# Kernel tuning notes

Measured on AMD Instinct MI355X. Metric: run time of the kernel, lower is better.

Reference implementation:

```python
import jax, jax.numpy as jnp
import numpy as np
from math import sqrt

D_MODEL, N_H, D_H, D_CQ, D_CKV, D_HR = 2048, 16, 128, 768, 512, 64
B, S = 1, 2048


def _rope_cos_sin(seq_len, dim, base=10000.0):
    inv_freq = 1.0 / (base ** (jnp.arange(0, dim, 2, dtype=jnp.float32) / dim))
    ang = jnp.arange(seq_len, dtype=jnp.float32)[:, None] * inv_freq[None, :]  # (S, dim//2)
    return jnp.cos(ang), jnp.sin(ang)


def _rope(t, cos, sin):
    # t: (B, S, ..., dim) with sequence on axis 1; interleaved complex pairs
    shp = t.shape
    d2 = shp[-1] // 2
    tr = t.reshape(shp[:-1] + (d2, 2))
    x0, x1 = tr[..., 0], tr[..., 1]
    bshape = (1, shp[1]) + (1,) * (x0.ndim - 3) + (d2,)
    cs, sn = cos.reshape(bshape), sin.reshape(bshape)
    return jnp.stack([x0 * cs - x1 * sn, x0 * sn + x1 * cs], axis=-1).reshape(shp)


def setup_inputs() -> dict:
    key = jax.random.key(0)
    ks = jax.random.split(key, 10)
    sc = 0.02
    inp = {
        "x": jax.random.normal(ks[0], (B, S, D_MODEL), jnp.float32),
        "mask": jnp.triu(jnp.ones((S, S), dtype=bool), k=1),  # True -> masked (causal)
        "w_norm": jnp.ones((D_MODEL,), jnp.float32),
        "w_cq": jax.random.normal(ks[1], (D_MODEL, D_CQ), jnp.float32) * sc,
        "w_q": jax.random.normal(ks[2], (D_CQ, N_H * D_H), jnp.float32) * sc,
        "w_qr": jax.random.normal(ks[3], (D_CQ, N_H * D_HR), jnp.float32) * sc,
        "w_ckv": jax.random.normal(ks[4], (D_MODEL, D_CKV), jnp.float32) * sc,
        "w_k": jax.random.normal(ks[5], (D_CKV, N_H * D_H), jnp.float32) * sc,
        "w_kr": jax.random.normal(ks[6], (D_MODEL, D_HR), jnp.float32) * sc,
        "w_v": jax.random.normal(ks[7], (D_CKV, D_MODEL), jnp.float32) * sc,
        "w_o": jax.random.normal(ks[8], (N_H * D_H, D_MODEL), jnp.float32) * sc,
    }
    return inp


def reference(x, mask, w_norm, w_cq, w_q, w_qr, w_ckv, w_k, w_kr, w_v, w_o):
    b, s, _ = x.shape
    eps = jnp.finfo(x.dtype).eps
    h = x * jax.lax.rsqrt(jnp.mean(x * x, axis=-1, keepdims=True) + eps) * w_norm  # RMSNorm
    cos, sin = _rope_cos_sin(s, D_HR)

    c_q = h @ w_cq  # (b, s, d_c_q)
    q_c = (c_q @ w_q).reshape(b, s, N_H, D_H).transpose(0, 2, 1, 3)          # (b, h, s, d_h)
    q_r = _rope((c_q @ w_qr).reshape(b, s, N_H, D_HR), cos, sin).transpose(0, 2, 1, 3)
    q = jnp.concatenate([q_c, q_r], axis=-1)  # (b, h, s, d_h + d_h_R)

    c_kv = h @ w_ckv  # (b, s, d_c_kv)
    k_c = (c_kv @ w_k).reshape(b, s, N_H, D_H).transpose(0, 2, 1, 3)
    k_r = _rope(h @ w_kr, cos, sin)[:, None]  # (b, 1, s, d_h_R), shared across heads
    k = jnp.concatenate([k_c, jnp.broadcast_to(k_r, (b, N_H, s, D_HR))], axis=-1)
    v = (c_kv @ w_v).reshape(b, s, N_H, D_H).transpose(0, 2, 1, 3)

    score = jnp.einsum('bhqd,bhkd->bhqk', q, k) / sqrt(D_H + D_HR)
    score = jnp.where(mask, -jnp.inf, score)
    attn = jax.nn.softmax(score, axis=-1)
    out = jnp.einsum('bhqk,bhkd->bhqd', attn, v)  # (b, h, s, d_h)
    out = out.transpose(0, 2, 1, 3).reshape(b, s, N_H * D_H) @ w_o
    return x + out
```

## Files before the change

### kernel.cpp

```cpp
#include <hip/hip_runtime.h>
#include <hip/hip_bf16.h>
#include <math.h>

#define D_MODEL 2048
#define N_H     16
#define D_H     128
#define D_CQ    768
#define D_CKV   512
#define D_HR    64
#define SEQ     2048
#define N_ACT1  1408
#define NSPLIT  4

typedef short bf16x8 __attribute__((ext_vector_type(8)));
typedef float f32x4  __attribute__((ext_vector_type(4)));

__device__ inline short f2bf(float f) {
  union { float f; unsigned u; } v; v.f = f;
  unsigned r = (v.u + 0x7fff + ((v.u >> 16) & 1)) >> 16;
  return (short)r;
}
__device__ inline float bf2f(short s) {
  union { float f; unsigned u; } v; v.u = ((unsigned)(unsigned short)s) << 16;
  return v.f;
}

__device__ inline void gld_lds16(const void* g, void* l) {
#if __has_builtin(__builtin_amdgcn_global_load_lds)
  __builtin_amdgcn_global_load_lds(
      (const __attribute__((address_space(1))) unsigned int*)g,
      (__attribute__((address_space(3))) unsigned int*)l, 16, 0, 0);
#else
  int lane = threadIdx.x & 63;
  *((uint4*)l + lane) = *(const uint4*)g;
#endif
}

__global__ __launch_bounds__(256) void rmsnorm_kernel(
    const float* __restrict__ x, const float* __restrict__ w,
    short* __restrict__ hb) {
  int row = blockIdx.x;
  int tid = threadIdx.x;
  const float* xr = x + (size_t)row * D_MODEL;
  float ss = 0.f;
  for (int i = tid; i < D_MODEL; i += 256) { float v = xr[i]; ss += v * v; }
  __shared__ float red[256];
  red[tid] = ss;
  __syncthreads();
  for (int s = 128; s > 0; s >>= 1) {
    if (tid < s) red[tid] += red[tid + s];
    __syncthreads();
  }
  float scale = rsqrtf(red[0] / (float)D_MODEL + 1.1920929e-7f);
  short* hbr = hb + (size_t)row * D_MODEL;
  for (int i = tid; i < D_MODEL; i += 256) hbr[i] = f2bf(xr[i] * scale * w[i]);
}

struct CastJobs {
  const float* src[8];
  short* dst[8];
  int K[8];
  int pref[9];
  int nx[8];
};

__global__ __launch_bounds__(256) void cast_all(CastJobs J) {
  int bid = blockIdx.x;
  int j = 0;
#pragma unroll
  for (int t = 0; t < 8; t++)
    if (bid >= J.pref[t + 1]) j = t + 1;
  int lid = bid - J.pref[j];
  int nx = J.nx[j];
  int ty = lid / nx, tx = lid - ty * nx;
  int n0 = tx * 64, k0 = ty * 64;
  int K = J.K[j];
  const float* W = J.src[j];
  short* Wt = J.dst[j];
  int Nfull = nx * 64;

  __shared__ short T[64][68];
  int tid = threadIdx.x;
#pragma unroll
  for (int it = 0; it < 16; it++) {
    int idx = it * 256 + tid;
    int r = idx >> 6, c = idx & 63;
    T[c][r] = f2bf(W[(size_t)(k0 + r) * Nfull + n0 + c]);
  }
  __syncthreads();
#pragma unroll
  for (int it = 0; it < 16; it++) {
    int idx = it * 256 + tid;
    int r = idx >> 6, c = idx & 63;
    Wt[(size_t)(n0 + r) * K + k0 + c] = T[r][c];
  }
}

__device__ __forceinline__ void gemm64_body(
    const short* __restrict__ A, const short* __restrict__ Bt,
    float* __restrict__ Cf, short* __restrict__ Cb, short* __restrict__ Cb2,
    const float* __restrict__ addv, int M, int N, int K, int lda, int mode,
    int bxx, int byy) {
  __shared__ short As[2 * 64 * 64];
  __shared__ short Bs[2 * 128 * 64];
  int tid = threadIdx.x;
  int w = tid >> 6, l = tid & 63;
  int lq = l >> 4, l16 = l & 15;
  int bm = byy * 64, bn = bxx * 128;
  int wr = w >> 1, wc = w & 1;
  int wm0 = wr * 32, wn0 = wc * 64;

  f32x4 acc[2][4];
#pragma unroll
  for (int i = 0; i < 2; i++)
#pragma unroll
    for (int j = 0; j < 4; j++) acc[i][j] = (f32x4)0.f;

  int rsub = (l >> 3);
  int csub = ((l & 7) ^ rsub) << 3;

  auto stage = [&](int buf, int k0) {
    short* Asb = As + buf * (64 * 64);
    short* Bsb = Bs + buf * (128 * 64);
#pragma unroll
    for (int i = 0; i < 2; i++) {
      int r0 = i * 32 + w * 8;
      gld_lds16(A + (size_t)(bm + r0 + rsub) * lda + k0 + csub, Asb + r0 * 64);
    }
#pragma unroll
    for (int i = 0; i < 4; i++) {
      int r0 = i * 32 + w * 8;
      gld_lds16(Bt + (size_t)(bn + r0 + rsub) * K + k0 + csub, Bsb + r0 * 64);
    }
  };

  stage(0, 0);
  int cur = 0;
  for (int k0 = 0; k0 < K; k0 += 64) {
    __syncthreads();
    if (k0 + 64 < K) stage(cur ^ 1, k0 + 64);
    const short* Asb = As + cur * (64 * 64);
    const short* Bsb = Bs + cur * (128 * 64);

#pragma unroll
    for (int ks = 0; ks < 2; ks++) {
      bf16x8 af[2], bfr[4];
      int sw = ((ks * 4 + lq) ^ (l16 & 7)) << 3;
#pragma unroll
      for (int mt = 0; mt < 2; mt++)
        af[mt] = *(const bf16x8*)&Asb[(wm0 + mt * 16 + l16) * 64 + sw];
#pragma unroll
      for (int nt = 0; nt < 4; nt++)
        bfr[nt] = *(const bf16x8*)&Bsb[(wn0 + nt * 16 + l16) * 64 + sw];
#pragma unroll
      for (int mt = 0; mt < 2; mt++)
#pragma unroll
        for (int nt = 0; nt < 4; nt++)
          acc[mt][nt] = __builtin_amdgcn_mfma_f32_16x16x32_bf16(af[mt], bfr[nt], acc[mt][nt], 0, 0, 0);
    }
    cur ^= 1;
  }

#pragma unroll
  for (int mt = 0; mt < 2; mt++)
#pragma unroll
    for (int i = 0; i < 4; i++) {
      int row = bm + wm0 + mt * 16 + lq * 4 + i;
#pragma unroll
      for (int nt = 0; nt < 4; nt++) {
        int col = bn + wn0 + nt * 16 + l16;
        float v = acc[mt][nt][i];
        if (mode == 0) {
          size_t off = (size_t)row * N + col;
          if (addv) v += addv[off];
          Cf[off] = v;
        } else if (mode == 1) {
          Cb[(size_t)row * N + col] = f2bf(v);
        } else if (mode == 3) {
          if (col < 2048) {
            Cb[((size_t)(col >> 7) * M + row) * 192 + (col & 127)] = f2bf(v);
          } else {
            int cc = col - 2048;
            int hh = cc >> 6, dd = cc & 63;
            float partner = __shfl_xor(v, 1);
            float inv = __expf(-((float)(dd & ~1) / 64.0f) * 9.210340372f);
            float ang = (float)row * inv;
            float c = __cosf(ang), s = __sinf(ang);
            float res = ((dd & 1) == 0) ? (v * c - partner * s)
                                        : (partner * s + v * c);
            Cb[((size_t)hh * M + row) * 192 + 128 + dd] = f2bf(res);
          }
        } else {
          if (col < 2048) {
            Cb[((size_t)(col >> 7) * M + row) * 192 + (col & 127)] = f2bf(v);
          } else {
            Cb2[(size_t)row * D_MODEL + (col - 2048)] = f2bf(v);
          }
        }
      }
    }
}

__global__ __launch_bounds__(256) void gemm_bf16_64(
    const short* __restrict__ A, const short* __restrict__ Bt,
    float* __restrict__ Cf, short* __restrict__ Cb, short* __restrict__ Cb2,
    const float* __restrict__ addv, int M, int N, int K, int lda, int mode) {
  gemm64_body(A, Bt, Cf, Cb, Cb2, addv, M, N, K, lda, mode,
              blockIdx.x, blockIdx.y);
}

__global__ __launch_bounds__(256) void gemm_qkv(
    const short* __restrict__ act1, const short* __restrict__ WT2,
    const short* __restrict__ WT3, short* __restrict__ qb,
    short* __restrict__ kb, short* __restrict__ vb) {
  int bx = blockIdx.x;
  if (bx < 24) {
    gemm64_body(act1, WT2, nullptr, qb, nullptr, nullptr,
                SEQ, 3072, D_CQ, N_ACT1, 3, bx, blockIdx.y);
  } else {
    gemm64_body(act1 + 768, WT3, nullptr, kb, vb, nullptr,
                SEQ, 4096, D_CKV, N_ACT1, 4, bx - 24, blockIdx.y);
  }
}

__global__ void rope_k_kernel(const short* __restrict__ act1, short* __restrict__ kb) {
  int idx = blockIdx.x * blockDim.x + threadIdx.x;
  if (idx >= SEQ * 32) return;
  int j = idx & 31;
  int s = idx >> 5;
  const short* p = act1 + (size_t)s * N_ACT1 + 1280 + 2 * j;
  float x0 = bf2f(p[0]), x1 = bf2f(p[1]);
  float inv = __expf(-((float)(2 * j) / 64.0f) * 9.210340372f);
  float ang = (float)s * inv;
  float c = __cosf(ang), sn = __sinf(ang);
  short b0 = f2bf(x0 * c - x1 * sn);
  short b1 = f2bf(x0 * sn + x1 * c);
#pragma unroll
  for (int hh = 0; hh < N_H; hh++) {
    short* k = kb + ((size_t)hh * SEQ + s) * 192 + 128 + 2 * j;
    k[0] = b0;
    k[1] = b1;
  }
}

__global__ __launch_bounds__(256) void cast_v_t(
    const short* __restrict__ vb, short* __restrict__ vt) {
  int s0 = blockIdx.x * 64;
  int h = blockIdx.y;
  __shared__ short T[128][72];
  int tid = threadIdx.x;
#pragma unroll
  for (int it = 0; it < 32; it++) {
    int c = it * 256 + tid;
    int r = c >> 7, d = c & 127;
    T[d][r] = vb[(size_t)(s0 + r) * D_MODEL + h * 128 + d];
  }
  __syncthreads();
#pragma unroll
  for (int it = 0; it < 32; it++) {
    int c = it * 256 + tid;
    int d = c >> 6, s = c & 63;
    vt[(size_t)(h * 128 + d) * SEQ + s0 + s] = T[d][s];
  }
}

#define TQ 128
#define TK 64

__global__ __launch_bounds__(256, 2) void attn_mfma(
    const short* __restrict__ qb, const short* __restrict__ kb,
    const short* __restrict__ vt, short* __restrict__ Opart,
    float* __restrict__ Lpart) {
  int bid = blockIdx.x;
  int h = bid & 15;
  int rest = bid >> 4;
  int qt = 15 - (rest / NSPLIT);
  int split = rest % NSPLIT;
  int q0 = qt * TQ;
  int nk = 2 * (qt + 1);
  int tid = threadIdx.x;
  int wave = tid >> 6, lane = tid & 63;
  int lq = lane >> 4, l16 = lane & 15;

  __shared__ short Ks[TK * 192];
  __shared__ short Vs[128 * 64];
  __shared__ short Ps[TQ * 64];

  bf16x8 qf[2][6];
  {
    const short* qp = qb + ((size_t)h * SEQ + q0 + wave * 32 + l16) * 192;
#pragma unroll
    for (int mt = 0; mt < 2; mt++)
#pragma unroll
      for (int ks = 0; ks < 6; ks++)
        qf[mt][ks] = *(const bf16x8*)(qp + (size_t)mt * 16 * 192 + ks * 32 + lq * 8);
  }

  bf16x8 ones;
#pragma unroll
  for (int i = 0; i < 8; i++) ones[i] = (short)0x3F80;

  f32x4 O[2][8];
  f32x4 Ol[2];
#pragma unroll
  for (int mt = 0; mt < 2; mt++) {
    Ol[mt] = (f32x4)0.f;
#pragma unroll
    for (int i = 0; i < 8; i++) O[mt][i] = (f32x4)0.f;
  }
  const float scale = 0.07216878364870323f;

  int goffK[6];
#pragma unroll
  for (int i = 0; i < 6; i++) {
    int s = i * 256 + tid;
    int r = s / 24;
    int c = s - r * 24;
    goffK[i] = r * 192 + ((c ^ (r & 7)) << 3);
  }
  int goffV[4];
  int vrow[4];
#pragma unroll
  for (int i = 0; i < 4; i++) {
    int s = i * 256 + tid;
    int d = s >> 3;
    int p = s & 7;
    vrow[i] = d;
    goffV[i] = (p ^ (d & 7)) << 3;
  }
  const short* kb_h = kb + (size_t)h * SEQ * 192;
  const short* vt_h = vt + (size_t)h * 128 * SEQ;

  auto stage_k = [&](int k0s) {
#pragma unroll
    for (int i = 0; i < 6; i++)
      gld_lds16(kb_h + (size_t)k0s * 192 + goffK[i],
                Ks + (size_t)(i * 256 + wave * 64) * 8);
  };
  auto stage_v = [&](int k0s) {
#pragma unroll
    for (int i = 0; i < 4; i++)
      gld_lds16(vt_h + (size_t)vrow[i] * SEQ + k0s + goffV[i],
                Vs + (size_t)(i * 256 + wave * 64) * 8);
  };

  if (split < nk) stage_k(split * TK);

  for (int t = split; t < nk; t += NSPLIT) {
    int k0 = t * TK;
    __syncthreads();

    stage_v(k0);

    f32x4 S[2][4];
#pragma unroll
    for (int mt = 0; mt < 2; mt++)
#pragma unroll
      for (int nt = 0; nt < 4; nt++) S[mt][nt] = (f32x4)0.f;
    __builtin_amdgcn_s_setprio(1);
#pragma unroll
    for (int ks = 0; ks < 6; ks++) {
#pragma unroll
      for (int nt = 0; nt < 4; nt++) {
        int row = nt * 16 + l16;
        bf16x8 b = *(const bf16x8*)&Ks[row * 192 +
                                       (((ks * 4 + lq) ^ (l16 & 7)) << 3)];
#pragma unroll
        for (int mt = 0; mt < 2; mt++)
          S[mt][nt] = __builtin_amdgcn_mfma_f32_16x16x32_bf16(qf[mt][ks], b, S[mt][nt], 0, 0, 0);
      }
    }
    __builtin_amdgcn_s_setprio(0);

#pragma unroll
    for (int mt = 0; mt < 2; mt++)
#pragma unroll
      for (int i = 0; i < 4; i++) {
        int pr = wave * 32 + mt * 16 + lq * 4 + i;
        int row = q0 + pr;
        bool may = (k0 + 63 > row);
#pragma unroll
        for (int nt = 0; nt < 4; nt++) {
          float p;
          if (may && (k0 + nt * 16 + l16 > row)) p = 0.f;
          else p = __expf(S[mt][nt][i] * scale);
          int j = nt * 16 + l16;
          Ps[pr * 64 + ((((j >> 3) ^ (pr & 7)) << 3) | (j & 7))] = f2bf(p);
        }
      }

    __syncthreads();

    if (t + NSPLIT < nk) stage_k((t + NSPLIT) * TK);

    __builtin_amdgcn_s_setprio(1);
#pragma unroll
    for (int kh = 0; kh < 2; kh++) {
      bf16x8 a[2];
#pragma unroll
      for (int mt = 0; mt < 2; mt++) {
        int prw = wave * 32 + mt * 16 + l16;
        a[mt] = *(const bf16x8*)&Ps[prw * 64 +
                                    (((kh * 4 + lq) ^ (l16 & 7)) << 3)];
        Ol[mt] = __builtin_amdgcn_mfma_f32_16x16x32_bf16(a[mt], ones, Ol[mt], 0, 0, 0);
      }
#pragma unroll
      for (int nt = 0; nt < 8; nt++) {
        int d = nt * 16 + l16;
        bf16x8 b = *(const bf16x8*)&Vs[d * 64 +
                                       (((kh * 4 + lq) ^ (d & 7)) << 3)];
#pragma unroll
        for (int mt = 0; mt < 2; mt++)
          O[mt][nt] = __builtin_amdgcn_mfma_f32_16x16x32_bf16(a[mt], b, O[mt][nt], 0, 0, 0);
      }
    }
    __builtin_amdgcn_s_setprio(0);
  }

#pragma unroll
  for (int mt = 0; mt < 2; mt++)
#pragma unroll
    for (int i = 0; i < 4; i++) {
      int row = q0 + wave * 32 + mt * 16 + lq * 4 + i;
      size_t base = ((size_t)(split * N_H + h) * SEQ + row);
      size_t obase = base * 128;
#pragma unroll
      for (int nt = 0; nt < 8; nt++)
        Opart[obase + nt * 16 + l16] = f2bf(O[mt][nt][i]);
      if (l16 == 0) Lpart[base] = Ol[mt][i];
    }
}

__global__ __launch_bounds__(256) void attn_merge(
    const short* __restrict__ Opart, const float* __restrict__ Lpart,
    short* __restrict__ aob) {
  int q0 = blockIdx.x * 16;
  int h = blockIdx.y;
  int tid = threadIdx.x;
#pragma unroll
  for (int i = 0; i < 8; i++) {
    int c = i * 256 + tid;
    int row = q0 + (c >> 7), d = c & 127;
    float denom = 0.f, num = 0.f;
#pragma unroll
    for (int p = 0; p < NSPLIT; p++) {
      size_t base = (size_t)(p * N_H + h) * SEQ + row;
      denom += Lpart[base];
      num += bf2f(Opart[base * 128 + d]);
    }
    aob[(size_t)row * D_MODEL + h * 128 + d] = f2bf(num / denom);
  }
}

extern "C" void kernel_launch(void* const* d_in, const int* in_sizes, int n_in,
                              void* d_out, int out_size, void* d_ws, size_t ws_size,
                              hipStream_t stream) {
  const float* x      = (const float*)d_in[0];
  const float* w_norm = (const float*)d_in[2];
  const float* w_cq   = (const float*)d_in[3];
  const float* w_q    = (const float*)d_in[4];
  const float* w_qr   = (const float*)d_in[5];
  const float* w_ckv  = (const float*)d_in[6];
  const float* w_k    = (const float*)d_in[7];
  const float* w_kr   = (const float*)d_in[8];
  const float* w_v    = (const float*)d_in[9];
  const float* w_o    = (const float*)d_in[10];
  float* out = (float*)d_out;

  char* ws = (char*)d_ws;
  short* h_bf  = (short*)ws;  ws += (size_t)SEQ * D_MODEL * 2;
  short* act1  = (short*)ws;  ws += (size_t)SEQ * N_ACT1 * 2;
  short* qb    = (short*)ws;  ws += (size_t)N_H * SEQ * 192 * 2;
  short* kb    = (short*)ws;  ws += (size_t)N_H * SEQ * 192 * 2;
  short* vb    = (short*)ws;  ws += (size_t)SEQ * D_MODEL * 2;
  short* vt    = (short*)ws;  ws += (size_t)SEQ * D_MODEL * 2;
  short* ao_bf = (short*)ws;  ws += (size_t)SEQ * D_MODEL * 2;
  short* Opart = (short*)ws;  ws += (size_t)NSPLIT * N_H * SEQ * 128 * 2;
  float* Lpart = (float*)ws;  ws += (size_t)NSPLIT * N_H * SEQ * 4;
  short* WT1   = (short*)ws;  ws += (size_t)N_ACT1 * D_MODEL * 2;
  short* WT2   = (short*)ws;  ws += (size_t)3072 * D_CQ * 2;
  short* WT3   = (short*)ws;  ws += (size_t)4096 * D_CKV * 2;
  short* WTO   = (short*)ws;  ws += (size_t)D_MODEL * D_MODEL * 2;

  CastJobs J;
  J.src[0] = w_cq;  J.dst[0] = WT1;                              J.K[0] = D_MODEL; J.nx[0] = D_CQ / 64;
  J.src[1] = w_ckv; J.dst[1] = WT1 + (size_t)768 * D_MODEL;      J.K[1] = D_MODEL; J.nx[1] = D_CKV / 64;
  J.src[2] = w_kr;  J.dst[2] = WT1 + (size_t)1280 * D_MODEL;     J.K[2] = D_MODEL; J.nx[2] = D_HR / 64;
  J.src[3] = w_q;   J.dst[3] = WT2;                              J.K[3] = D_CQ;    J.nx[3] = 2048 / 64;
  J.src[4] = w_qr;  J.dst[4] = WT2 + (size_t)2048 * D_CQ;        J.K[4] = D_CQ;    J.nx[4] = 1024 / 64;
  J.src[5] = w_k;   J.dst[5] = WT3;                              J.K[5] = D_CKV;   J.nx[5] = 2048 / 64;
  J.src[6] = w_v;   J.dst[6] = WT3 + (size_t)2048 * D_CKV;       J.K[6] = D_CKV;   J.nx[6] = 2048 / 64;
  J.src[7] = w_o;   J.dst[7] = WTO;                              J.K[7] = D_MODEL; J.nx[7] = 2048 / 64;
  int pref = 0;
  for (int j = 0; j < 8; j++) {
    J.pref[j] = pref;
    pref += J.nx[j] * (J.K[j] / 64);
  }
  J.pref[8] = pref;
  cast_all<<<pref, 256, 0, stream>>>(J);

  rmsnorm_kernel<<<SEQ, 256, 0, stream>>>(x, w_norm, h_bf);

  gemm_bf16_64<<<dim3(N_ACT1 / 128, SEQ / 64), 256, 0, stream>>>(
      h_bf, WT1, nullptr, act1, nullptr, nullptr, SEQ, N_ACT1, D_MODEL, D_MODEL, 1);

  rope_k_kernel<<<(SEQ * 32 + 255) / 256, 256, 0, stream>>>(act1, kb);

  gemm_qkv<<<dim3(24 + 32, SEQ / 64), 256, 0, stream>>>(
      act1, WT2, WT3, qb, kb, vb);

  cast_v_t<<<dim3(SEQ / 64, N_H), 256, 0, stream>>>(vb, vt);

  attn_mfma<<<dim3((SEQ / TQ) * NSPLIT * N_H), 256, 0, stream>>>(qb, kb, vt, Opart, Lpart);
  attn_merge<<<dim3(SEQ / 16, N_H), 256, 0, stream>>>(Opart, Lpart, ao_bf);

  gemm_bf16_64<<<dim3(D_MODEL / 128, SEQ / 64), 256, 0, stream>>>(
      ao_bf, WTO, out, nullptr, nullptr, x, SEQ, D_MODEL, D_MODEL, D_MODEL, 0);
}
```

Measured before the change: 300.5 us.

## Fuse rmsnorm into weight-cast kernel and split-K the output projection GEMM

The rmsnorm work is folded into the weight-cast launch as extra blocks, which removes one kernel launch and lets the two jobs run side by side. The final output projection is split along K into two halves, so the grid has twice as many workgroups and fills more of the GPU. The two fp32 partials are written into the reused Opart buffer, and a separate merge kernel adds them together with the residual x. The split adds extra fp32 partial traffic and one more launch, and a leading-dimension parameter is added to the GEMM body so it can handle the K-slices.

Measured after the change: 306.1 us. Within noise of the previous version (+1.9%).

```diff
diff --git a/kernel.cpp b/kernel.cpp
--- a/kernel.cpp
+++ b/kernel.cpp
@@ -36,26 +36,6 @@
 #endif
 }
 
-__global__ __launch_bounds__(256) void rmsnorm_kernel(
-    const float* __restrict__ x, const float* __restrict__ w,
-    short* __restrict__ hb) {
-  int row = blockIdx.x;
-  int tid = threadIdx.x;
-  const float* xr = x + (size_t)row * D_MODEL;
-  float ss = 0.f;
-  for (int i = tid; i < D_MODEL; i += 256) { float v = xr[i]; ss += v * v; }
-  __shared__ float red[256];
-  red[tid] = ss;
-  __syncthreads();
-  for (int s = 128; s > 0; s >>= 1) {
-    if (tid < s) red[tid] += red[tid + s];
-    __syncthreads();
-  }
-  float scale = rsqrtf(red[0] / (float)D_MODEL + 1.1920929e-7f);
-  short* hbr = hb + (size_t)row * D_MODEL;
-  for (int i = tid; i < D_MODEL; i += 256) hbr[i] = f2bf(xr[i] * scale * w[i]);
-}
-
 struct CastJobs {
   const float* src[8];
   short* dst[8];
@@ -64,8 +44,30 @@
   int nx[8];
 };
 
-__global__ __launch_bounds__(256) void cast_all(CastJobs J) {
+__global__ __launch_bounds__(256) void prep_all(
+    CastJobs J, const float* __restrict__ x, const float* __restrict__ wn,
+    short* __restrict__ hb) {
   int bid = blockIdx.x;
+  int tid = threadIdx.x;
+
+  if (bid >= J.pref[8]) {
+    int row = bid - J.pref[8];
+    const float* xr = x + (size_t)row * D_MODEL;
+    float ss = 0.f;
+    for (int i = tid; i < D_MODEL; i += 256) { float v = xr[i]; ss += v * v; }
+    __shared__ float red[256];
+    red[tid] = ss;
+    __syncthreads();
+    for (int s = 128; s > 0; s >>= 1) {
+      if (tid < s) red[tid] += red[tid + s];
+      __syncthreads();
+    }
+    float scale = rsqrtf(red[0] / (float)D_MODEL + 1.1920929e-7f);
+    short* hbr = hb + (size_t)row * D_MODEL;
+    for (int i = tid; i < D_MODEL; i += 256) hbr[i] = f2bf(xr[i] * scale * wn[i]);
+    return;
+  }
+
   int j = 0;
 #pragma unroll
   for (int t = 0; t < 8; t++)
@@ -80,7 +82,6 @@
   int Nfull = nx * 64;
 
   __shared__ short T[64][68];
-  int tid = threadIdx.x;
 #pragma unroll
   for (int it = 0; it < 16; it++) {
     int idx = it * 256 + tid;
@@ -99,8 +100,8 @@
 __device__ __forceinline__ void gemm64_body(
     const short* __restrict__ A, const short* __restrict__ Bt,
     float* __restrict__ Cf, short* __restrict__ Cb, short* __restrict__ Cb2,
-    const float* __restrict__ addv, int M, int N, int K, int lda, int mode,
-    int bxx, int byy) {
+    const float* __restrict__ addv, int M, int N, int K, int lda, int ldb,
+    int mode, int bxx, int byy) {
   __shared__ short As[2 * 64 * 64];
   __shared__ short Bs[2 * 128 * 64];
   int tid = threadIdx.x;
@@ -130,7 +131,7 @@
 #pragma unroll
     for (int i = 0; i < 4; i++) {
       int r0 = i * 32 + w * 8;
-      gld_lds16(Bt + (size_t)(bn + r0 + rsub) * K + k0 + csub, Bsb + r0 * 64);
+      gld_lds16(Bt + (size_t)(bn + r0 + rsub) * ldb + k0 + csub, Bsb + r0 * 64);
     }
   };
 
@@ -204,8 +205,9 @@
 __global__ __launch_bounds__(256) void gemm_bf16_64(
     const short* __restrict__ A, const short* __restrict__ Bt,
     float* __restrict__ Cf, short* __restrict__ Cb, short* __restrict__ Cb2,
-    const float* __restrict__ addv, int M, int N, int K, int lda, int mode) {
-  gemm64_body(A, Bt, Cf, Cb, Cb2, addv, M, N, K, lda, mode,
+    const float* __restrict__ addv, int M, int N, int K, int lda, int ldb,
+    int mode) {
+  gemm64_body(A, Bt, Cf, Cb, Cb2, addv, M, N, K, lda, ldb, mode,
               blockIdx.x, blockIdx.y);
 }
 
@@ -216,11 +218,35 @@
   int bx = blockIdx.x;
   if (bx < 24) {
     gemm64_body(act1, WT2, nullptr, qb, nullptr, nullptr,
-                SEQ, 3072, D_CQ, N_ACT1, 3, bx, blockIdx.y);
+                SEQ, 3072, D_CQ, N_ACT1, D_CQ, 3, bx, blockIdx.y);
   } else {
     gemm64_body(act1 + 768, WT3, nullptr, kb, vb, nullptr,
-                SEQ, 4096, D_CKV, N_ACT1, 4, bx - 24, blockIdx.y);
-  }
+                SEQ, 4096, D_CKV, N_ACT1, D_CKV, 4, bx - 24, blockIdx.y);
+  }
+}
+
+__global__ __launch_bounds__(256) void gemm_fin_split(
+    const short* __restrict__ A, const short* __restrict__ Bt,
+    float* __restrict__ P) {
+  int z = blockIdx.z;
+  gemm64_body(A + z * 1024, Bt + z * 1024, P + (size_t)z * SEQ * D_MODEL,
+              nullptr, nullptr, nullptr, SEQ, D_MODEL, 1024, D_MODEL, D_MODEL,
+              0, blockIdx.x, blockIdx.y);
+}
+
+__global__ __launch_bounds__(256) void gemm_fin_merge(
+    const float* __restrict__ P, const float* __restrict__ x,
+    float* __restrict__ out) {
+  size_t i = ((size_t)blockIdx.x * 256 + threadIdx.x) * 4;
+  float4 a = *(const float4*)(P + i);
+  float4 b = *(const float4*)(P + (size_t)SEQ * D_MODEL + i);
+  float4 c = *(const float4*)(x + i);
+  float4 o;
+  o.x = a.x + b.x + c.x;
+  o.y = a.y + b.y + c.y;
+  o.z = a.z + b.z + c.z;
+  o.w = a.w + b.w + c.w;
+  *(float4*)(out + i) = o;
 }
 
 __global__ void rope_k_kernel(const short* __restrict__ act1, short* __restrict__ kb) {
@@ -482,6 +508,8 @@
   short* WT3   = (short*)ws;  ws += (size_t)4096 * D_CKV * 2;
   short* WTO   = (short*)ws;  ws += (size_t)D_MODEL * D_MODEL * 2;
 
+  float* Pfin = (float*)Opart;
+
   CastJobs J;
   J.src[0] = w_cq;  J.dst[0] = WT1;                              J.K[0] = D_MODEL; J.nx[0] = D_CQ / 64;
   J.src[1] = w_ckv; J.dst[1] = WT1 + (size_t)768 * D_MODEL;      J.K[1] = D_MODEL; J.nx[1] = D_CKV / 64;
@@ -497,12 +525,11 @@
     pref += J.nx[j] * (J.K[j] / 64);
   }
   J.pref[8] = pref;
-  cast_all<<<pref, 256, 0, stream>>>(J);
-
-  rmsnorm_kernel<<<SEQ, 256, 0, stream>>>(x, w_norm, h_bf);
+  prep_all<<<pref + SEQ, 256, 0, stream>>>(J, x, w_norm, h_bf);
 
   gemm_bf16_64<<<dim3(N_ACT1 / 128, SEQ / 64), 256, 0, stream>>>(
-      h_bf, WT1, nullptr, act1, nullptr, nullptr, SEQ, N_ACT1, D_MODEL, D_MODEL, 1);
+      h_bf, WT1, nullptr, act1, nullptr, nullptr, SEQ, N_ACT1, D_MODEL,
+      D_MODEL, D_MODEL, 1);
 
   rope_k_kernel<<<(SEQ * 32 + 255) / 256, 256, 0, stream>>>(act1, kb);
 
@@ -514,6 +541,8 @@
   attn_mfma<<<dim3((SEQ / TQ) * NSPLIT * N_H), 256, 0, stream>>>(qb, kb, vt, Opart, Lpart);
   attn_merge<<<dim3(SEQ / 16, N_H), 256, 0, stream>>>(Opart, Lpart, ao_bf);
 
-  gemm_bf16_64<<<dim3(D_MODEL / 128, SEQ / 64), 256, 0, stream>>>(
-      ao_bf, WTO, out, nullptr, nullptr, x, SEQ, D_MODEL, D_MODEL, D_MODEL, 0);
-}
+  gemm_fin_split<<<dim3(D_MODEL / 128, SEQ / 64, 2), 256, 0, stream>>>(
+      ao_bf, WTO, Pfin);
+  gemm_fin_merge<<<(SEQ * D_MODEL) / (256 * 4), 256, 0, stream>>>(
+      Pfin, x, out);
+}
```
